# Performance work log

Measured on AMD Instinct MI355X. Metric: run time of the kernel, lower is better.

The kernel has to match this reference:

```python
import jax, jax.numpy as jnp
import numpy as np

N_FEATURES = 1024
N_HEADS = 16
D_ATTN = 64


def setup_inputs() -> dict:
    key = jax.random.key(0)
    k_x, k_qkv, k_pw, k_pb = jax.random.split(key, 4)
    B, S = 2, 2048
    x = jax.random.normal(k_x, (B, S, N_FEATURES), dtype=jnp.float32)
    # torch nn.Linear weights are [out, in]; init scale ~ 1/sqrt(in)
    w_qkv = jax.random.normal(k_qkv, (3 * N_HEADS * D_ATTN, N_FEATURES), dtype=jnp.float32) / np.sqrt(N_FEATURES)
    w_proj = jax.random.normal(k_pw, (N_FEATURES, N_HEADS * D_ATTN), dtype=jnp.float32) / np.sqrt(N_HEADS * D_ATTN)
    b_proj = jax.random.normal(k_pb, (N_FEATURES,), dtype=jnp.float32) / np.sqrt(N_HEADS * D_ATTN)
    return {"x": x, "w_qkv": w_qkv, "w_proj": w_proj, "b_proj": b_proj}


def reference(x, w_qkv, w_proj, b_proj):
    B, S, F = x.shape
    H, D = N_HEADS, D_ATTN
    # fused QKV projection (bias=False): [B,S,3*H*D]
    qkv = jnp.einsum('bsf,of->bso', x, w_qkv)
    qkv = qkv.reshape(B, S, 3, H, D)
    q = jnp.transpose(qkv[:, :, 0], (0, 2, 1, 3))  # [B,H,S,D]
    k = jnp.transpose(qkv[:, :, 1], (0, 2, 1, 3))
    v = jnp.transpose(qkv[:, :, 2], (0, 2, 1, 3))
    scale = 1.0 / jnp.sqrt(jnp.asarray(D, dtype=x.dtype))
    scores = jnp.einsum('bhqd,bhkd->bhqk', q, k) * scale  # [B,H,S,S]
    attn = jax.nn.softmax(scores, axis=-1)
    out = jnp.einsum('bhqk,bhkd->bhqd', attn, v)  # [B,H,S,D]
    out = jnp.transpose(out, (0, 2, 1, 3)).reshape(B, S, H * D)
    # output projection (dropout is identity in eval mode)
    return jnp.einsum('bsm,fm->bsf', out, w_proj) + b_proj
```

## Files before the change

kernel.cpp:

```cpp
#include <hip/hip_runtime.h>
#include <hip/hip_bf16.h>
#include <math.h>

#define BATCH 2
#define SEQ 2048
#define NFEAT 1024
#define NHEAD 16
#define DHEAD 64
#define MROWS (BATCH * SEQ)
#define NQKV (3 * NHEAD * DHEAD)

typedef __attribute__((ext_vector_type(8))) short short8;
typedef __attribute__((ext_vector_type(4))) float floatx4;
typedef __attribute__((ext_vector_type(16))) float floatx16;
typedef __attribute__((ext_vector_type(4))) unsigned int uintx4;

#define CEXP 0.18033688f

__device__ __forceinline__ unsigned short f2bf(float f) {
    unsigned int u = __float_as_uint(f);
    u += 0x7fff + ((u >> 16) & 1);
    return (unsigned short)(u >> 16);
}

__device__ __forceinline__ float fast_exp2(float x) {
    return __builtin_amdgcn_exp2f(x);
}

__device__ __forceinline__ uint pack_bf16x2(float lo, float hi) {
    float2 t; t.x = lo; t.y = hi;
    __hip_bfloat162 h = __float22bfloat162_rn(t);
    union { __hip_bfloat162 h; uint u; } c; c.h = h;
    return c.u;
}

__device__ __forceinline__ void async16(const void* g, void* l) {
    __builtin_amdgcn_global_load_lds(
        (const __attribute__((address_space(1))) void*)g,
        (__attribute__((address_space(3))) void*)l, 16, 0, 0);
}

__global__ void cvt_swz(const float* __restrict__ x, const float* __restrict__ wq,
                        const float* __restrict__ wp,
                        ushort* __restrict__ xb, ushort* __restrict__ wqb,
                        ushort* __restrict__ wpb) {
    const int NX = MROWS * NFEAT / 4, NWQ = NQKV * NFEAT / 4, NWP = NFEAT * NFEAT / 4;
    int i = blockIdx.x * blockDim.x + threadIdx.x;
    if (i >= NX + NWQ + NWP) return;
    const float* src; ushort* dst; int idx4;
    if (i < NX)            { src = x;  dst = xb;  idx4 = i; }
    else if (i < NX + NWQ) { src = wq; dst = wqb; idx4 = i - NX; }
    else                   { src = wp; dst = wpb; idx4 = i - NX - NWQ; }
    float4 v = ((const float4*)src)[idx4];
    ushort4 o;
    o.x = f2bf(v.x); o.y = f2bf(v.y); o.z = f2bf(v.z); o.w = f2bf(v.w);
    const int e = idx4 * 4;
    const int k = e & (NFEAT - 1);
    const int row = e >> 10;
    const int kp = (k & ~31) | (((((k >> 3) & 3) ^ ((row >> 1) & 3))) << 3) | (k & 7);
    *(ushort4*)(dst + (size_t)row * NFEAT + kp) = o;
}

__global__ __launch_bounds__(256, 3)
void gemm_qkv(const ushort* __restrict__ A, const ushort* __restrict__ W,
              ushort* __restrict__ qb, ushort* __restrict__ kb, ushort* __restrict__ vtb) {
    __shared__ ushort smem[16384];
    ushort* As = smem;
    ushort* Bs = smem + 8192;
    const int tid = threadIdx.x;
    const int wave = tid >> 6, lane = tid & 63;
    const int id = blockIdx.x;
    const int xcd = id & 7, slot = id >> 3;
    const int by = (xcd >> 1) * 8 + slot / 12;
    const int bx = (xcd & 1) * 12 + slot % 12;
    const int m0 = by * 128, n0 = bx * 128;
    const int wm = (wave >> 1) * 64, wn = (wave & 1) * 64;
    const int lr = lane & 15, lg = lane >> 4;
    const int kswz = (lg ^ ((lr >> 1) & 3)) * 8;

    floatx4 acc[4][4] = {};

    for (int k0 = 0; k0 < NFEAT; k0 += 64) {
#pragma unroll
        for (int q = 0; q < 4; ++q) {
            const int s = q * 256 + tid;
            const int row = s >> 3, kc = (s & 7) * 8;
            async16(A + (size_t)(m0 + row) * NFEAT + k0 + kc, (void*)(As + s * 8));
            async16(W + (size_t)(n0 + row) * NFEAT + k0 + kc, (void*)(Bs + s * 8));
        }
        __syncthreads();
#pragma unroll
        for (int kk = 0; kk < 2; ++kk) {
            short8 a[4], b[4];
#pragma unroll
            for (int i = 0; i < 4; ++i)
                a[i] = *(const short8*)(As + (wm + i * 16 + lr) * 64 + kk * 32 + kswz);
#pragma unroll
            for (int j = 0; j < 4; ++j)
                b[j] = *(const short8*)(Bs + (wn + j * 16 + lr) * 64 + kk * 32 + kswz);
#pragma unroll
            for (int i = 0; i < 4; ++i)
#pragma unroll
                for (int j = 0; j < 4; ++j)
                    acc[i][j] = __builtin_amdgcn_mfma_f32_16x16x32_bf16(a[i], b[j], acc[i][j], 0, 0, 0);
        }
        __syncthreads();
    }

    const int t = n0 >> 10;
    const int bidx = m0 >> 11;
    if (t < 2) {
#pragma unroll
        for (int i = 0; i < 4; ++i)
#pragma unroll
            for (int j = 0; j < 4; ++j)
#pragma unroll
                for (int r = 0; r < 4; ++r) {
                    const int m = m0 + wm + i * 16 + lg * 4 + r;
                    const int n = n0 + wn + j * 16 + lr;
                    const int s = m & (SEQ - 1);
                    const int rem = n & 1023, h = rem >> 6, d = rem & 63;
                    if (t == 0) {
                        qb[((size_t)(bidx * NHEAD + h) * SEQ + s) * DHEAD + d] =
                            f2bf(acc[i][j][r] * CEXP);
                    } else {
                        const int dcol = ((((d >> 3) ^ (s & 7)) << 3)) | (d & 7);
                        kb[((size_t)(bidx * NHEAD + h) * SEQ + s) * DHEAD + dcol] =
                            f2bf(acc[i][j][r]);
                    }
                }
    } else {
#pragma unroll
        for (int hhalf = 0; hhalf < 2; ++hhalf) {
            if ((wm >> 6) == hhalf) {
#pragma unroll
                for (int i = 0; i < 4; ++i) {
                    const int chunk = i * 2 + (lg >> 1);
#pragma unroll
                    for (int j = 0; j < 4; ++j) {
                        const int n = wn + j * 16 + lr;
                        uint2 pk;
                        pk.x = pack_bf16x2(acc[i][j][0], acc[i][j][1]);
                        pk.y = pack_bf16x2(acc[i][j][2], acc[i][j][3]);
                        *(uint2*)(smem + n * 64 + ((chunk ^ (n & 7)) * 8) + (lg & 1) * 4) = pk;
                    }
                }
            }
            __syncthreads();
            const int s_base = (m0 & (SEQ - 1)) + hhalf * 64;
#pragma unroll
            for (int it = 0; it < 4; ++it) {
                const int n_r = (tid >> 3) + it * 32;
                const int p = tid & 7;
                short8 rowv = *(const short8*)(smem + n_r * 64 + p * 8);
                const int nglob = n0 + n_r;
                const int d = nglob & 63, hh = (nglob & 1023) >> 6;
                *(short8*)(vtb + ((size_t)(bidx * NHEAD + hh) * DHEAD + d) * SEQ + s_base + p * 8) = rowv;
            }
            __syncthreads();
        }
    }
}

__global__ __launch_bounds__(256, 2)
void gemm_proj(const ushort* __restrict__ A, const ushort* __restrict__ W,
               const float* __restrict__ bias, float* __restrict__ Cout) {
    __shared__ ushort As[128 * 64];
    __shared__ ushort Bs[64 * 64];
    const int tid = threadIdx.x;
    const int wave = tid >> 6, lane = tid & 63;
    const int id = blockIdx.x;
    const int xcd = id & 7, slot = id >> 3;
    const int by = (xcd >> 1) * 8 + (slot >> 3);
    const int bx = (xcd & 1) * 8 + (slot & 7);
    const int m0 = by * 128, n0 = bx * 64;
    const int wm = (wave >> 1) * 64, wn = (wave & 1) * 32;
    const int lr = lane & 15, lg = lane >> 4;
    const int kswz = (lg ^ ((lr >> 1) & 3)) * 8;

    floatx4 acc[4][2] = {};

    for (int k0 = 0; k0 < NFEAT; k0 += 64) {
#pragma unroll
        for (int q = 0; q < 4; ++q) {
            const int s = q * 256 + tid;
            const int row = s >> 3, kc = (s & 7) * 8;
            async16(A + (size_t)(m0 + row) * NFEAT + k0 + kc, (void*)(As + s * 8));
        }
#pragma unroll
        for (int q = 0; q < 2; ++q) {
            const int s = q * 256 + tid;
            const int row = s >> 3, kc = (s & 7) * 8;
            async16(W + (size_t)(n0 + row) * NFEAT + k0 + kc, (void*)(Bs + s * 8));
        }
        __syncthreads();
#pragma unroll
        for (int kk = 0; kk < 2; ++kk) {
            short8 a[4], b[2];
#pragma unroll
            for (int i = 0; i < 4; ++i)
                a[i] = *(const short8*)(As + (wm + i * 16 + lr) * 64 + kk * 32 + kswz);
#pragma unroll
            for (int j = 0; j < 2; ++j)
                b[j] = *(const short8*)(Bs + (wn + j * 16 + lr) * 64 + kk * 32 + kswz);
#pragma unroll
            for (int i = 0; i < 4; ++i)
#pragma unroll
                for (int j = 0; j < 2; ++j)
                    acc[i][j] = __builtin_amdgcn_mfma_f32_16x16x32_bf16(a[i], b[j], acc[i][j], 0, 0, 0);
        }
        __syncthreads();
    }

#pragma unroll
    for (int i = 0; i < 4; ++i)
#pragma unroll
        for (int j = 0; j < 2; ++j)
#pragma unroll
            for (int r = 0; r < 4; ++r) {
                const int m = m0 + wm + i * 16 + lg * 4 + r;
                const int n = n0 + wn + j * 16 + lr;
                Cout[(size_t)m * NFEAT + n] = acc[i][j][r] + bias[n];
            }
}

__global__ __launch_bounds__(512, 4)
void flash_attn(const ushort* __restrict__ qb, const ushort* __restrict__ kb,
                const ushort* __restrict__ vtb, ushort* __restrict__ aob) {
    const int id = blockIdx.x;
    const int xcd = id & 7, slot = id >> 3;
    const int bh = xcd + 8 * (slot >> 4);
    const int qt = slot & 15;
    const int tid = threadIdx.x, wave = tid >> 6, lane = tid & 63;
    const int l31 = lane & 31, l5 = lane >> 5;
    const int swz = lane & 7;
    const int kvh = wave >> 2;
    const int qw = wave & 3;

    __shared__ ushort Ks[2][2][64 * 64];
    __shared__ ushort Vs[2][2][64 * 64];

    const ushort* Qb = qb + (size_t)bh * SEQ * DHEAD;
    const ushort* Kb = kb + (size_t)bh * SEQ * DHEAD;
    const ushort* Vt = vtb + (size_t)bh * DHEAD * SEQ;

    const int q0 = qt * 128 + qw * 32;

    short8 qf[4];
#pragma unroll
    for (int kw = 0; kw < 4; ++kw)
        qf[kw] = *(const short8*)(Qb + (size_t)(q0 + l31) * DHEAD + kw * 16 + l5 * 8);

    const int kofs = tid * 8;
    const size_t vrow = (size_t)(tid >> 3) * SEQ;
    const int vcol = (tid & 7) * 8;

    const ushort* KsW = &Ks[kvh][0][0];
    const ushort* VsW = &Vs[kvh][0][0];

    floatx16 acc_o[2] = {};
    float l_lane = 0.0f;

#define FLASH_PREFETCH(BUF, KV)                                                     \
    {                                                                               \
        const int kv_ = (KV);                                                       \
        async16(Kb + (size_t)kv_ * DHEAD + kofs,            (void*)(Ks[0][BUF] + kofs)); \
        async16(Kb + (size_t)(1024 + kv_) * DHEAD + kofs,   (void*)(Ks[1][BUF] + kofs)); \
        async16(Vt + vrow + kv_ + vcol,                     (void*)(Vs[0][BUF] + kofs)); \
        async16(Vt + vrow + 1024 + kv_ + vcol,              (void*)(Vs[1][BUF] + kofs)); \
    }

#define FLASH_COMPUTE(BUF)                                                          \
    {                                                                               \
        floatx16 st[2] = {};                                                        \
        __builtin_amdgcn_s_setprio(1);                                              \
        _Pragma("unroll")                                                           \
        for (int kw = 0; kw < 4; ++kw) {                                            \
            _Pragma("unroll")                                                       \
            for (int i = 0; i < 2; ++i) {                                           \
                short8 kf = *(const short8*)(KsW + (BUF) * 4096 + (i * 32 + l31) * 64 + \
                                             (((kw * 2 + l5) ^ swz) * 8));          \
                st[i] = __builtin_amdgcn_mfma_f32_32x32x16_bf16(kf, qf[kw], st[i], 0, 0, 0); \
            }                                                                       \
        }                                                                           \
        __builtin_amdgcn_s_setprio(0);                                              \
        uintx4 pa[4];                                                               \
        _Pragma("unroll")                                                           \
        for (int i = 0; i < 2; ++i) {                                               \
            uint P2[8];                                                             \
            _Pragma("unroll")                                                       \
            for (int rr = 0; rr < 8; ++rr) {                                        \
                const float p0 = fast_exp2(st[i][rr * 2]);                          \
                const float p1 = fast_exp2(st[i][rr * 2 + 1]);                      \
                l_lane += p0 + p1;                                                  \
                P2[rr] = pack_bf16x2(p0, p1);                                       \
            }                                                                       \
            _Pragma("unroll")                                                       \
            for (int r3 = 0; r3 < 2; ++r3) {                                        \
                _Pragma("unroll")                                                   \
                for (int r1 = 0; r1 < 2; ++r1) {                                    \
                    uint a = P2[r3 * 4 + r1];                            \
                    uint b = P2[r3 * 4 + 2 + r1];                        \
                    asm volatile("v_permlane32_swap_b32 %0, %1" : "+v"(a), "+v"(b)); \
                    pa[i * 2 + r3][r1] = a;               \
                    pa[i * 2 + r3][2 + r1] = b;           \
                }                                                                   \
            }                                                                       \
        }                                                                           \
        __builtin_amdgcn_s_setprio(1);                                              \
        _Pragma("unroll")                                                           \
        for (int kk = 0; kk < 4; ++kk) {                                            \
            const short8 paf = *(const short8*)&pa[kk];                             \
            _Pragma("unroll")                                                       \
            for (int j2 = 0; j2 < 2; ++j2) {                                        \
                short8 vf = *(const short8*)(VsW + (BUF) * 4096 + (j2 * 32 + l31) * 64 + \
                                             (((kk * 2 + l5) ^ swz) * 8));          \
                acc_o[j2] = __builtin_amdgcn_mfma_f32_32x32x16_bf16(paf, vf, acc_o[j2], 0, 0, 0); \
            }                                                                       \
        }                                                                           \
        __builtin_amdgcn_s_setprio(0);                                              \
    }

    FLASH_PREFETCH(0, 0)

    for (int kt = 0; kt < 1024; kt += 128) {
        __syncthreads();
        FLASH_PREFETCH(1, kt + 64)
        FLASH_COMPUTE(0)
        __syncthreads();
        if (kt + 128 < 1024)
            FLASH_PREFETCH(0, kt + 128)
        FLASH_COMPUTE(1)
    }
#undef FLASH_PREFETCH
#undef FLASH_COMPUTE

    __syncthreads();
    float* mrg = (float*)&Ks[0][0][0];
    if (wave >= 4) {
        float* p = mrg + (size_t)(wave - 4) * 2304 + lane * 36;
#pragma unroll
        for (int j2 = 0; j2 < 2; ++j2)
#pragma unroll
            for (int r4 = 0; r4 < 4; ++r4) {
                floatx4 v;
                v[0] = acc_o[j2][r4 * 4 + 0];
                v[1] = acc_o[j2][r4 * 4 + 1];
                v[2] = acc_o[j2][r4 * 4 + 2];
                v[3] = acc_o[j2][r4 * 4 + 3];
                *(floatx4*)(p + j2 * 16 + r4 * 4) = v;
            }
        p[32] = l_lane;
    }
    __syncthreads();
    if (wave < 4) {
        const float* p = mrg + (size_t)wave * 2304 + lane * 36;
#pragma unroll
        for (int j2 = 0; j2 < 2; ++j2)
#pragma unroll
            for (int r4 = 0; r4 < 4; ++r4) {
                floatx4 v = *(const floatx4*)(p + j2 * 16 + r4 * 4);
#pragma unroll
                for (int e = 0; e < 4; ++e)
                    acc_o[j2][r4 * 4 + e] += v[e];
            }
        l_lane += p[32];

        l_lane += __shfl_xor(l_lane, 32);
        const float invl = 1.0f / l_lane;

        const int b = bh >> 4, h = bh & 15;
#pragma unroll
        for (int r = 0; r < 16; ++r) {
            const int qrow = (r & 3) + 4 * l5 + 8 * (r >> 2);
            const float il = __shfl(invl, qrow);
            const int srow = b * SEQ + q0 + qrow;
            const int key = (srow >> 1) & 3;
#pragma unroll
            for (int j2 = 0; j2 < 2; ++j2) {
                const int d = j2 * 32 + l31;
                const int dsw = (d & ~31) | ((((d >> 3) & 3) ^ key) << 3) | (d & 7);
                aob[(size_t)srow * (NHEAD * DHEAD) + h * DHEAD + dsw] = f2bf(acc_o[j2][r] * il);
            }
        }
    }
}

extern "C" void kernel_launch(void* const* d_in, const int* in_sizes, int n_in,
                              void* d_out, int out_size, void* d_ws, size_t ws_size,
                              hipStream_t stream) {
    const float* x      = (const float*)d_in[0];
    const float* w_qkv  = (const float*)d_in[1];
    const float* w_proj = (const float*)d_in[2];
    const float* b_proj = (const float*)d_in[3];
    float* out = (float*)d_out;

    ushort* ws = (ushort*)d_ws;
    ushort* xb     = ws;
    ushort* wqkvb  = xb + (size_t)MROWS * NFEAT;
    ushort* wprojb = wqkvb + (size_t)NQKV * NFEAT;
    ushort* qb     = wprojb + (size_t)NFEAT * NFEAT;
    ushort* kb     = qb + (size_t)MROWS * NFEAT;
    ushort* vtb    = kb + (size_t)MROWS * NFEAT;
    ushort* aob    = vtb + (size_t)MROWS * NFEAT;

    {
        const int total = (MROWS * NFEAT + NQKV * NFEAT + NFEAT * NFEAT) / 4;
        cvt_swz<<<(total + 255) / 256, 256, 0, stream>>>(x, w_qkv, w_proj, xb, wqkvb, wprojb);
    }

    {
        gemm_qkv<<<768, 256, 0, stream>>>(xb, wqkvb, qb, kb, vtb);
    }

    {
        flash_attn<<<512, 512, 0, stream>>>(qb, kb, vtb, aob);
    }

    {
        gemm_proj<<<512, 256, 0, stream>>>(aob, wprojb, b_proj, out);
    }
}
```

Baseline: 176.2 us.

## Use raw barriers with partial vmcnt waits in flash attention; enlarge proj GEMM tiles

The flash attention loop swaps __syncthreads for raw s_barrier plus explicit vmcnt(4) waits, so the prefetch of the next K/V buffer can stay in flight while the current one is consumed. It also splits the row-sum accumulation into two partial sums to shorten the dependency chain, and flattens shared memory into a single array. The output projection GEMM moves to 128x128 tiles with 512 threads and half as many blocks, to get more reuse per block. The risk is fragile hand-written wait counts, and fewer blocks in the proj GEMM may leave CUs underused.

```diff
diff --git a/kernel.cpp b/kernel.cpp
--- a/kernel.cpp
+++ b/kernel.cpp
@@ -39,6 +39,10 @@
         (const __attribute__((address_space(1))) void*)g,
         (__attribute__((address_space(3))) void*)l, 16, 0, 0);
 }
+
+#define BAR_RAW() asm volatile("s_barrier" ::: "memory")
+#define WAITV4()  { asm volatile("s_waitcnt vmcnt(4)" ::: "memory"); __builtin_amdgcn_sched_barrier(0); }
+#define WAITV0()  { asm volatile("s_waitcnt vmcnt(0)" ::: "memory"); __builtin_amdgcn_sched_barrier(0); }
 
 __global__ void cvt_swz(const float* __restrict__ x, const float* __restrict__ wq,
                         const float* __restrict__ wp,
@@ -162,60 +166,55 @@
     }
 }
 
-__global__ __launch_bounds__(256, 2)
+__global__ __launch_bounds__(512, 2)
 void gemm_proj(const ushort* __restrict__ A, const ushort* __restrict__ W,
                const float* __restrict__ bias, float* __restrict__ Cout) {
     __shared__ ushort As[128 * 64];
-    __shared__ ushort Bs[64 * 64];
+    __shared__ ushort Bs[128 * 64];
     const int tid = threadIdx.x;
     const int wave = tid >> 6, lane = tid & 63;
     const int id = blockIdx.x;
     const int xcd = id & 7, slot = id >> 3;
-    const int by = (xcd >> 1) * 8 + (slot >> 3);
-    const int bx = (xcd & 1) * 8 + (slot & 7);
-    const int m0 = by * 128, n0 = bx * 64;
-    const int wm = (wave >> 1) * 64, wn = (wave & 1) * 32;
+    const int by = xcd * 4 + (slot >> 3);
+    const int bx = slot & 7;
+    const int m0 = by * 128, n0 = bx * 128;
+    const int wm = (wave >> 1) * 32, wn = (wave & 1) * 64;
     const int lr = lane & 15, lg = lane >> 4;
     const int kswz = (lg ^ ((lr >> 1) & 3)) * 8;
 
-    floatx4 acc[4][2] = {};
+    floatx4 acc[2][4] = {};
 
     for (int k0 = 0; k0 < NFEAT; k0 += 64) {
 #pragma unroll
-        for (int q = 0; q < 4; ++q) {
-            const int s = q * 256 + tid;
+        for (int q = 0; q < 2; ++q) {
+            const int s = q * 512 + tid;
             const int row = s >> 3, kc = (s & 7) * 8;
             async16(A + (size_t)(m0 + row) * NFEAT + k0 + kc, (void*)(As + s * 8));
-        }
-#pragma unroll
-        for (int q = 0; q < 2; ++q) {
-            const int s = q * 256 + tid;
-            const int row = s >> 3, kc = (s & 7) * 8;
             async16(W + (size_t)(n0 + row) * NFEAT + k0 + kc, (void*)(Bs + s * 8));
         }
         __syncthreads();
 #pragma unroll
         for (int kk = 0; kk < 2; ++kk) {
-            short8 a[4], b[2];
-#pragma unroll
-            for (int i = 0; i < 4; ++i)
+            short8 a[2], b[4];
+#pragma unroll
+            for (int i = 0; i < 2; ++i)
                 a[i] = *(const short8*)(As + (wm + i * 16 + lr) * 64 + kk * 32 + kswz);
 #pragma unroll
-            for (int j = 0; j < 2; ++j)
+            for (int j = 0; j < 4; ++j)
                 b[j] = *(const short8*)(Bs + (wn + j * 16 + lr) * 64 + kk * 32 + kswz);
 #pragma unroll
-            for (int i = 0; i < 4; ++i)
-#pragma unroll
-                for (int j = 0; j < 2; ++j)
+            for (int i = 0; i < 2; ++i)
+#pragma unroll
+                for (int j = 0; j < 4; ++j)
                     acc[i][j] = __builtin_amdgcn_mfma_f32_16x16x32_bf16(a[i], b[j], acc[i][j], 0, 0, 0);
         }
         __syncthreads();
     }
 
 #pragma unroll
-    for (int i = 0; i < 4; ++i)
-#pragma unroll
-        for (int j = 0; j < 2; ++j)
+    for (int i = 0; i < 2; ++i)
+#pragma unroll
+        for (int j = 0; j < 4; ++j)
 #pragma unroll
             for (int r = 0; r < 4; ++r) {
                 const int m = m0 + wm + i * 16 + lg * 4 + r;
@@ -233,12 +232,13 @@
     const int qt = slot & 15;
     const int tid = threadIdx.x, wave = tid >> 6, lane = tid & 63;
     const int l31 = lane & 31, l5 = lane >> 5;
-    const int swz = lane & 7;
+    const int swz = l31 & 7;
     const int kvh = wave >> 2;
     const int qw = wave & 3;
 
-    __shared__ ushort Ks[2][2][64 * 64];
-    __shared__ ushort Vs[2][2][64 * 64];
+    __shared__ __align__(16) ushort sm[32768];
+    ushort* Ksp = sm;
+    ushort* Vsp = sm + 16384;
 
     const ushort* Qb = qb + (size_t)bh * SEQ * DHEAD;
     const ushort* Kb = kb + (size_t)bh * SEQ * DHEAD;
@@ -255,8 +255,8 @@
     const size_t vrow = (size_t)(tid >> 3) * SEQ;
     const int vcol = (tid & 7) * 8;
 
-    const ushort* KsW = &Ks[kvh][0][0];
-    const ushort* VsW = &Vs[kvh][0][0];
+    const ushort* KsW = Ksp + kvh * 8192;
+    const ushort* VsW = Vsp + kvh * 8192;
 
     floatx16 acc_o[2] = {};
     float l_lane = 0.0f;
@@ -264,10 +264,10 @@
 #define FLASH_PREFETCH(BUF, KV)                                                     \
     {                                                                               \
         const int kv_ = (KV);                                                       \
-        async16(Kb + (size_t)kv_ * DHEAD + kofs,            (void*)(Ks[0][BUF] + kofs)); \
-        async16(Kb + (size_t)(1024 + kv_) * DHEAD + kofs,   (void*)(Ks[1][BUF] + kofs)); \
-        async16(Vt + vrow + kv_ + vcol,                     (void*)(Vs[0][BUF] + kofs)); \
-        async16(Vt + vrow + 1024 + kv_ + vcol,              (void*)(Vs[1][BUF] + kofs)); \
+        async16(Kb + (size_t)kv_ * DHEAD + kofs,          (void*)(Ksp + (BUF) * 4096 + kofs));        \
+        async16(Kb + (size_t)(1024 + kv_) * DHEAD + kofs, (void*)(Ksp + 8192 + (BUF) * 4096 + kofs)); \
+        async16(Vt + vrow + kv_ + vcol,                   (void*)(Vsp + (BUF) * 4096 + kofs));        \
+        async16(Vt + vrow + 1024 + kv_ + vcol,            (void*)(Vsp + 8192 + (BUF) * 4096 + kofs)); \
     }
 
 #define FLASH_COMPUTE(BUF)                                                          \
@@ -288,13 +288,15 @@
         _Pragma("unroll")                                                           \
         for (int i = 0; i < 2; ++i) {                                               \
             uint P2[8];                                                             \
+            float lsA = 0.0f, lsB = 0.0f;                                           \
             _Pragma("unroll")                                                       \
             for (int rr = 0; rr < 8; ++rr) {                                        \
                 const float p0 = fast_exp2(st[i][rr * 2]);                          \
                 const float p1 = fast_exp2(st[i][rr * 2 + 1]);                      \
-                l_lane += p0 + p1;                                                  \
+                if (rr & 1) lsB += p0 + p1; else lsA += p0 + p1;                    \
                 P2[rr] = pack_bf16x2(p0, p1);                                       \
             }                                                                       \
+            l_lane += lsA + lsB;                                                    \
             _Pragma("unroll")                                                       \
             for (int r3 = 0; r3 < 2; ++r3) {                                        \
                 _Pragma("unroll")                                                   \
@@ -324,21 +326,28 @@
     FLASH_PREFETCH(0, 0)
 
     for (int kt = 0; kt < 1024; kt += 128) {
-        __syncthreads();
+        BAR_RAW();
         FLASH_PREFETCH(1, kt + 64)
+        WAITV4();
+        BAR_RAW();
         FLASH_COMPUTE(0)
-        __syncthreads();
-        if (kt + 128 < 1024)
+        BAR_RAW();
+        if (kt + 128 < 1024) {
             FLASH_PREFETCH(0, kt + 128)
+            WAITV4();
+        } else {
+            WAITV0();
+        }
+        BAR_RAW();
         FLASH_COMPUTE(1)
     }
 #undef FLASH_PREFETCH
 #undef FLASH_COMPUTE
 
     __syncthreads();
-    float* mrg = (float*)&Ks[0][0][0];
-    if (wave >= 4) {
-        float* p = mrg + (size_t)(wave - 4) * 2304 + lane * 36;
+    float* mrg = (float*)sm;
+    float* p = mrg + (size_t)(qw * 64 + lane) * 36;
+    if (kvh == 1) {
 #pragma unroll
         for (int j2 = 0; j2 < 2; ++j2)
 #pragma unroll
@@ -353,8 +362,7 @@
         p[32] = l_lane;
     }
     __syncthreads();
-    if (wave < 4) {
-        const float* p = mrg + (size_t)wave * 2304 + lane * 36;
+    if (kvh == 0) {
 #pragma unroll
         for (int j2 = 0; j2 < 2; ++j2)
 #pragma unroll
@@ -418,6 +426,6 @@
     }
 
     {
-        gemm_proj<<<512, 256, 0, stream>>>(aob, wprojb, b_proj, out);
-    }
-}
+        gemm_proj<<<256, 512, 0, stream>>>(aob, wprojb, b_proj, out);
+    }
+}
```

Measured after the change: 177.8 us. No clear change (+0.9%).
